# Optimization experiments

Measured on AMD Instinct MI355X. Metric: run time of the kernel, lower is better.

## Reference

```python
import jax, jax.numpy as jnp
import numpy as np

DIM = 768
NUM_HEADS = 12
HEAD_DIM = DIM // NUM_HEADS
SCALE = HEAD_DIM ** -0.5
H_IN, W_IN = 14, 14
N_TOK = H_IN * W_IN + 1  # 197 (patches + cls)
NUM_REL = (2 * H_IN - 1) * (2 * W_IN - 1) + 3  # 732
B = 128


def _build_rel_index():
    coords = np.stack(np.meshgrid(np.arange(H_IN), np.arange(W_IN), indexing='ij'))  # (2,H,W)
    flat = coords.reshape(2, -1)  # (2, H*W)
    rel = flat[:, :, None] - flat[:, None, :]  # (2, HW, HW)
    rel = rel.transpose(1, 2, 0).astype(np.int64)  # (HW, HW, 2)
    rel[:, :, 0] += H_IN - 1
    rel[:, :, 1] += W_IN - 1
    rel[:, :, 0] *= 2 * W_IN - 1
    idx = np.zeros((N_TOK, N_TOK), dtype=np.int64)
    idx[1:, 1:] = rel.sum(-1)
    idx[0, :] = NUM_REL - 3
    idx[:, 0] = NUM_REL - 2
    idx[0, 0] = NUM_REL - 1
    return jnp.asarray(idx, dtype=jnp.int32)


def binarize(x):
    # forward of STESign: -1 if x<0 else 1 (sign(0)->1)
    return jnp.where(x >= 0, 1.0, -1.0).astype(x.dtype)


def quantize_qk(x):
    # per-(B,H) mean-abs scale over token and head_dim axes, times sign
    s = jnp.mean(jnp.abs(x), axis=(-2, -1), keepdims=True)
    return s * binarize(x)


def round_ste(z):
    return z + jax.lax.stop_gradient(jnp.round(z) - z)


def quantize_p(x):
    qmax = 255.0
    s = 1.0 / qmax
    q = jnp.clip(round_ste(x / s), 0.0, qmax)
    return s * q


def quantize_v(x):
    # symmetric 8-bit quantization, channelwise over last dim, clip [-2,2]
    clipped = jnp.clip(x, -2.0, 2.0)
    max_in = jnp.max(jnp.abs(clipped), axis=-1, keepdims=True)
    s = (2.0 ** 7 - 1.0) / (max_in + 1e-8)
    return jnp.round(clipped * s) / s


def setup_inputs() -> dict:
    key = jax.random.key(0)
    ks = jax.random.split(key, 5)
    x = jax.random.normal(ks[0], (B, N_TOK, DIM), dtype=jnp.float32)
    qkv_w = jax.random.normal(ks[1], (3 * DIM, DIM), dtype=jnp.float32) * (DIM ** -0.5)
    proj_w = jax.random.normal(ks[2], (DIM, DIM), dtype=jnp.float32) * (DIM ** -0.5)
    proj_b = jnp.zeros((DIM,), dtype=jnp.float32)
    rel_bias_table = jax.random.normal(ks[3], (NUM_REL, NUM_HEADS), dtype=jnp.float32) * 0.02
    rel_index = _build_rel_index()
    return {"x": x, "qkv_w": qkv_w, "proj_w": proj_w, "proj_b": proj_b,
            "rel_bias_table": rel_bias_table, "rel_index": rel_index}


def reference(x, qkv_w, proj_w, proj_b, rel_bias_table, rel_index):
    Bsz, N, C = x.shape
    qkv = x @ qkv_w.T  # (B,N,3C)
    qkv = qkv.reshape(Bsz, N, 3, NUM_HEADS, HEAD_DIM)
    qkv = jnp.transpose(qkv, (2, 0, 3, 1, 4))  # (3,B,H,N,hd)
    q, k, v = qkv[0], qkv[1], qkv[2]
    q = quantize_qk(q)
    k = quantize_qk(k)
    attn = jnp.einsum('bhnd,bhmd->bhnm', q, k) * SCALE  # (B,H,N,N)
    bias = rel_bias_table[rel_index]  # (N,N,H)
    attn = attn + jnp.transpose(bias, (2, 0, 1))[None]
    attn = jax.nn.softmax(attn, axis=-1)
    attn = quantize_p(attn)
    v = quantize_v(v)
    out = jnp.einsum('bhnm,bhmd->bhnd', attn, v)  # (B,H,N,hd)
    out = jnp.transpose(out, (0, 2, 1, 3)).reshape(Bsz, N, C)
    out = out @ proj_w.T + proj_b
    return out
```

## Files before the change

kernel.cpp:

```cpp
#include <hip/hip_runtime.h>
#include <cstdint>
#include <cmath>

#define NTOK 197
#define NHEAD 12
#define HD 64
#define CDIM 768
#define KPZ 200
#define VTS 256

typedef __attribute__((ext_vector_type(8))) short short8v;
typedef __attribute__((ext_vector_type(8))) _Float16 half8v;
typedef __attribute__((ext_vector_type(4))) float f32x4;

__device__ __forceinline__ unsigned short f2bf(float f) {
  unsigned u = __builtin_bit_cast(unsigned, f);
  unsigned r = (u + 0x7fffu + ((u >> 16) & 1u)) >> 16;
  return (unsigned short)r;
}
__device__ __forceinline__ float bf2f(unsigned short h) {
  unsigned u = ((unsigned)h) << 16;
  return __builtin_bit_cast(float, u);
}

__device__ __forceinline__ void gload_lds16(const unsigned short* g, unsigned short* l) {
  __builtin_amdgcn_global_load_lds(
      (const __attribute__((address_space(1))) unsigned int*)(const void*)g,
      (__attribute__((address_space(3))) unsigned int*)(void*)l, 16, 0, 0);
}

__global__ __launch_bounds__(256) void bias_pre_kernel(
    const float* __restrict__ table, const int* __restrict__ relidx,
    float* __restrict__ bias_pre, int total)
{
  int i = blockIdx.x * 256 + threadIdx.x;
  if (i >= total) return;
  int nm = i % (NTOK * NTOK);
  int h  = i / (NTOK * NTOK);
  bias_pre[i] = table[relidx[nm] * NHEAD + h];
}

__global__ __launch_bounds__(256) void split2h_kernel(
    const float* __restrict__ src,
    unsigned short* __restrict__ d0, unsigned short* __restrict__ d1,
    int Mreal, int C, long long total4)
{
  long long idx = (long long)blockIdx.x * 256 + threadIdx.x;
  if (idx >= total4) return;
  long long e = idx * 4;
  int r = (int)(e / C);
  float4 v = make_float4(0.f, 0.f, 0.f, 0.f);
  if (r < Mreal) v = *(const float4*)(src + e);
  const float vv[4] = {v.x, v.y, v.z, v.w};
  ushort4 o0, o1;
  unsigned short* p0 = (unsigned short*)&o0;
  unsigned short* p1 = (unsigned short*)&o1;
#pragma unroll
  for (int i = 0; i < 4; ++i) {
    const float t = vv[i] * 64.0f;
    const _Float16 h0 = (_Float16)t;
    const float rr = t - (float)h0;
    const _Float16 h1 = (_Float16)(rr * 4096.0f);
    p0[i] = __builtin_bit_cast(unsigned short, h0);
    p1[i] = __builtin_bit_cast(unsigned short, h1);
  }
  *(ushort4*)(d0 + e) = o0;
  *(ushort4*)(d1 + e) = o1;
}

template <int BANDW>
__global__ __launch_bounds__(256, 3) void gemm_f16(
    const unsigned short* __restrict__ A, size_t aplane,
    const unsigned short* __restrict__ B, size_t bplane,
    const float* __restrict__ bias, float* __restrict__ C,
    int M, int N, int K)
{
  __shared__ unsigned short Asm[2][128][64];
  __shared__ unsigned short Bsm[2][64][64];

  const int nwg = gridDim.x;
  const int orig = blockIdx.x;
  const int q = nwg >> 3, r = nwg & 7;
  const int xcd = orig & 7, pos = orig >> 3;
  const int wg = (xcd < r ? xcd * (q + 1) : r * (q + 1) + (xcd - r) * q) + pos;
  const int byCount = (M + 127) >> 7;
  const int bandSz = byCount * BANDW;
  const int band = wg / bandSz;
  const int rem = wg % bandSz;
  const int by = rem / BANDW;
  const int bx = band * BANDW + rem % BANDW;
  const int bm = by * 128, bn = bx * 64;

  const int tid = threadIdx.x;
  const int w = tid >> 6, lane = tid & 63;
  const int wr = w >> 1, wc = w & 1;
  const int srow = tid >> 3;
  const int sslot = tid & 7;
  const int sgW = (sslot ^ (srow & 7)) * 8;
  const int fr = lane & 15;
  const int fq = lane >> 4;
  const int mrow = wr * 64 + fr;
  const int ncol = wc * 32;
  const int kc0 = 8 * ((fq) ^ (fr & 7));
  const int kc1 = 8 * ((4 + fq) ^ (fr & 7));

  size_t aoffs[4], boffs[2];
#pragma unroll
  for (int ps = 0; ps < 4; ++ps) aoffs[ps] = (size_t)(bm + srow + 32 * ps) * K + sgW;
#pragma unroll
  for (int ps = 0; ps < 2; ++ps) boffs[ps] = (size_t)(bn + srow + 32 * ps) * K + sgW;

  f32x4 accA[4][2], accB[4][2];
#pragma unroll
  for (int i = 0; i < 4; ++i)
#pragma unroll
    for (int j = 0; j < 2; ++j) {
      accA[i][j] = (f32x4){0.f, 0.f, 0.f, 0.f};
      accB[i][j] = (f32x4){0.f, 0.f, 0.f, 0.f};
    }

  auto stage = [&](int k0) {
#pragma unroll
    for (int ps = 0; ps < 4; ++ps) {
      const int dr = srow + 32 * ps;
      gload_lds16(A + aoffs[ps] + k0,          &Asm[0][dr][sslot * 8]);
      gload_lds16(A + aplane + aoffs[ps] + k0, &Asm[1][dr][sslot * 8]);
    }
#pragma unroll
    for (int ps = 0; ps < 2; ++ps) {
      const int dr = srow + 32 * ps;
      gload_lds16(B + boffs[ps] + k0,          &Bsm[0][dr][sslot * 8]);
      gload_lds16(B + bplane + boffs[ps] + k0, &Bsm[1][dr][sslot * 8]);
    }
  };

  stage(0);
  __syncthreads();

#pragma unroll 1
  for (int k0 = 0; k0 < K; k0 += 64) {
    {
      half8v b0[2], b1[2];
#pragma unroll
      for (int nt = 0; nt < 2; ++nt) {
        b0[nt] = *(const half8v*)&Bsm[0][ncol + nt * 16 + fr][kc0];
        b1[nt] = *(const half8v*)&Bsm[1][ncol + nt * 16 + fr][kc0];
      }
#pragma unroll
      for (int mt = 0; mt < 4; ++mt) {
        const half8v a0 = *(const half8v*)&Asm[0][mrow + mt * 16][kc0];
        const half8v a1 = *(const half8v*)&Asm[1][mrow + mt * 16][kc0];
#pragma unroll
        for (int nt = 0; nt < 2; ++nt)
          accA[mt][nt] = __builtin_amdgcn_mfma_f32_16x16x32_f16(
              a0, b0[nt], accA[mt][nt], 0, 0, 0);
#pragma unroll
        for (int nt = 0; nt < 2; ++nt)
          accB[mt][nt] = __builtin_amdgcn_mfma_f32_16x16x32_f16(
              a0, b1[nt], accB[mt][nt], 0, 0, 0);
#pragma unroll
        for (int nt = 0; nt < 2; ++nt)
          accB[mt][nt] = __builtin_amdgcn_mfma_f32_16x16x32_f16(
              a1, b0[nt], accB[mt][nt], 0, 0, 0);
      }
    }
    {
      half8v a0[4], a1[4], b0[2], b1[2];
#pragma unroll
      for (int mt = 0; mt < 4; ++mt) {
        a0[mt] = *(const half8v*)&Asm[0][mrow + mt * 16][kc1];
        a1[mt] = *(const half8v*)&Asm[1][mrow + mt * 16][kc1];
      }
#pragma unroll
      for (int nt = 0; nt < 2; ++nt) {
        b0[nt] = *(const half8v*)&Bsm[0][ncol + nt * 16 + fr][kc1];
        b1[nt] = *(const half8v*)&Bsm[1][ncol + nt * 16 + fr][kc1];
      }
      __syncthreads();
      if (k0 + 64 < K) stage(k0 + 64);
      __builtin_amdgcn_sched_barrier(0);
#pragma unroll
      for (int mt = 0; mt < 4; ++mt)
#pragma unroll
        for (int nt = 0; nt < 2; ++nt)
          accA[mt][nt] = __builtin_amdgcn_mfma_f32_16x16x32_f16(
              a0[mt], b0[nt], accA[mt][nt], 0, 0, 0);
#pragma unroll
      for (int mt = 0; mt < 4; ++mt)
#pragma unroll
        for (int nt = 0; nt < 2; ++nt)
          accB[mt][nt] = __builtin_amdgcn_mfma_f32_16x16x32_f16(
              a0[mt], b1[nt], accB[mt][nt], 0, 0, 0);
#pragma unroll
      for (int mt = 0; mt < 4; ++mt)
#pragma unroll
        for (int nt = 0; nt < 2; ++nt)
          accB[mt][nt] = __builtin_amdgcn_mfma_f32_16x16x32_f16(
              a1[mt], b0[nt], accB[mt][nt], 0, 0, 0);
    }
    __syncthreads();
  }

  constexpr float S1 = 1.0f / 4096.0f;
#pragma unroll
  for (int nt = 0; nt < 2; ++nt) {
    const int col = bn + wc * 32 + nt * 16 + fr;
    const float bcol = bias ? bias[col] : 0.0f;
#pragma unroll
    for (int mt = 0; mt < 4; ++mt) {
      const int rowbase = bm + wr * 64 + mt * 16 + fq * 4;
#pragma unroll
      for (int j = 0; j < 4; ++j) {
        const int row = rowbase + j;
        if (row < M)
          C[(size_t)row * N + col] =
              (accA[mt][nt][j] + accB[mt][nt][j] * S1) * S1 + bcol;
      }
    }
  }
}

__global__ __launch_bounds__(512, 4) void attn_kernel(
    const float* __restrict__ qkv, const float* __restrict__ bias_pre,
    unsigned short* __restrict__ att0, unsigned short* __restrict__ att1)
{
  __shared__ unsigned short vT[2][HD][VTS];
  __shared__ unsigned char  zb[32][KPZ];
  __shared__ unsigned long long qb[200];
  __shared__ unsigned long long kbt[200];
  __shared__ float red[16];

  const int bh = blockIdx.x;
  const int b = bh / NHEAD;
  const int h = bh % NHEAD;
  const int tid = threadIdx.x;
  const int w = tid >> 6;
  const int lane = tid & 63;
  const float* base = qkv + (size_t)b * (NTOK * 3 * CDIM) + h * HD;

  float sq = 0.f, sk = 0.f;
  for (int n = w; n < NTOK; n += 8) {
    const float* row = base + (size_t)n * (3 * CDIM);
    const float qv = row[lane];
    const float kv = row[CDIM + lane];
    const float vv = row[2 * CDIM + lane];
    sq += fabsf(qv);
    sk += fabsf(kv);
    const unsigned long long qm = __ballot(qv >= 0.0f);
    const unsigned long long km = __ballot(kv >= 0.0f);
    if (lane == 0) { qb[n] = qm; kbt[n] = km; }
    const float c = fminf(fmaxf(vv, -2.0f), 2.0f);
    float a = fabsf(c);
#pragma unroll
    for (int off = 32; off; off >>= 1) a = fmaxf(a, __shfl_xor(a, off));
    const float s = 127.0f / (a + 1e-8f);
    const float vq = rintf(c * s) / s;
    const unsigned short l0 = f2bf(vq);
    const unsigned short l1 = f2bf(vq - bf2f(l0));
    const int gsw = ((((n >> 3) ^ (lane & 31)) << 3) | (n & 7));
    vT[0][lane][gsw] = l0;
    vT[1][lane][gsw] = l1;
  }
#pragma unroll
  for (int off = 32; off; off >>= 1) {
    sq += __shfl_xor(sq, off);
    sk += __shfl_xor(sk, off);
  }
  if (lane == 0) { red[w] = sq; red[8 + w] = sk; }
  __syncthreads();
  float s_q = 0.f, s_k = 0.f;
#pragma unroll
  for (int i = 0; i < 8; ++i) { s_q += red[i]; s_k += red[8 + i]; }
  s_q *= (1.0f / (NTOK * HD));
  s_k *= (1.0f / (NTOK * HD));
  const float coef = s_q * s_k * 0.125f;

  const float* biash = bias_pre + (size_t)h * (NTOK * NTOK);
  const float SP = 1.0f / 255.0f;

  const int mt = w >> 2;
  const int nt = w & 3;
  const int arow = mt * 16 + (lane & 15);
  const int bcol = nt * 16 + (lane & 15);
  const int kq8 = 8 * (lane >> 4);
  const int rowb = mt * 16 + ((lane >> 4) << 2);
  const int colOut = h * HD + bcol;
  const int bsw = bcol & 31;

  for (int g = 0; g < 7; ++g) {
    const int r0 = g * 32;

#pragma unroll
    for (int i = 0; i < 4; ++i) {
      const int r = r0 + w * 4 + i;
      if (r < NTOK) {
        const unsigned long long qn = qb[r];
        const float* brow = biash + (size_t)r * NTOK;
        float lg[4];
#pragma unroll
        for (int t = 0; t < 4; ++t) {
          const int m = lane + t * 64;
          if (m < NTOK) {
            const int dot = 64 - 2 * __popcll(qn ^ kbt[m]);
            lg[t] = fmaf(coef, (float)dot, brow[m]);
          } else {
            lg[t] = -INFINITY;
          }
        }
        float mx = fmaxf(fmaxf(lg[0], lg[1]), fmaxf(lg[2], lg[3]));
#pragma unroll
        for (int off = 32; off; off >>= 1) mx = fmaxf(mx, __shfl_xor(mx, off));
        const float p0 = expf(lg[0] - mx);
        const float p1 = expf(lg[1] - mx);
        const float p2 = expf(lg[2] - mx);
        const float p3 = expf(lg[3] - mx);
        float sum = p0 + p1 + p2 + p3;
#pragma unroll
        for (int off = 32; off; off >>= 1) sum += __shfl_xor(sum, off);
        float z0 = rintf((p0 / sum) / SP); z0 = fminf(fmaxf(z0, 0.f), 255.f);
        float z1 = rintf((p1 / sum) / SP); z1 = fminf(fmaxf(z1, 0.f), 255.f);
        float z2 = rintf((p2 / sum) / SP); z2 = fminf(fmaxf(z2, 0.f), 255.f);
        float z3 = rintf((p3 / sum) / SP); z3 = fminf(fmaxf(z3, 0.f), 255.f);
        const int zr = w * 4 + i;
        zb[zr][lane]       = (unsigned char)(int)z0;
        zb[zr][lane + 64]  = (unsigned char)(int)z1;
        zb[zr][lane + 128] = (unsigned char)(int)z2;
        if (lane + 192 < NTOK) zb[zr][lane + 192] = (unsigned char)(int)z3;
      }
    }
    __syncthreads();

    f32x4 acc = (f32x4){0.f, 0.f, 0.f, 0.f};
#pragma unroll
    for (int k0 = 0; k0 < 192; k0 += 32) {
      const unsigned long long a8 =
          *(const unsigned long long*)&zb[arow][k0 + kq8];
      short8v af;
#pragma unroll
      for (int j = 0; j < 8; ++j) {
        const float f = (float)((unsigned)(a8 >> (8 * j)) & 0xFFu);
        af[j] = (short)(__builtin_bit_cast(unsigned, f) >> 16);
      }
      const int kg = (((k0 + kq8) >> 3) ^ bsw) << 3;
      const short8v b0 = *(const short8v*)&vT[0][bcol][kg];
      const short8v b1 = *(const short8v*)&vT[1][bcol][kg];
      acc = __builtin_amdgcn_mfma_f32_16x16x32_bf16(af, b0, acc, 0, 0, 0);
      acc = __builtin_amdgcn_mfma_f32_16x16x32_bf16(af, b1, acc, 0, 0, 0);
    }
#pragma unroll
    for (int j = 0; j < 4; ++j) {
      float a = acc[j];
#pragma unroll
      for (int m = 192; m < 197; ++m) {
        const int mg = ((((m >> 3) ^ bsw) << 3) | (m & 7));
        const float zv = (float)zb[rowb + j][m];
        const float vv = bf2f(vT[0][bcol][mg]) + bf2f(vT[1][bcol][mg]);
        a = fmaf(zv, vv, a);
      }
      acc[j] = a;
    }
#pragma unroll
    for (int j = 0; j < 4; ++j) {
      const int row = r0 + rowb + j;
      if (row < NTOK) {
        const size_t off = ((size_t)b * NTOK + row) * CDIM + colOut;
        const float t = acc[j] * SP * 64.0f;
        const _Float16 h0 = (_Float16)t;
        const float rr = t - (float)h0;
        const _Float16 h1 = (_Float16)(rr * 4096.0f);
        att0[off] = __builtin_bit_cast(unsigned short, h0);
        att1[off] = __builtin_bit_cast(unsigned short, h1);
      }
    }
    __syncthreads();
  }
}

extern "C" void kernel_launch(void* const* d_in, const int* in_sizes, int n_in,
                              void* d_out, int out_size, void* d_ws, size_t ws_size,
                              hipStream_t stream)
{
  (void)in_sizes; (void)n_in; (void)out_size;
  const float* x      = (const float*)d_in[0];
  const float* qkv_w  = (const float*)d_in[1];
  const float* proj_w = (const float*)d_in[2];
  const float* proj_b = (const float*)d_in[3];
  const float* table  = (const float*)d_in[4];
  const int*   relidx = (const int*)d_in[5];
  float* out = (float*)d_out;

  const size_t biasElems = (size_t)NHEAD * NTOK * NTOK;
  const size_t wqPlane = (size_t)(3 * CDIM) * CDIM;
  const size_t wpPlane = (size_t)CDIM * CDIM;

  int nb = 128;
  size_t Mpad = 0;
  for (;; nb >>= 1) {
    size_t Mreal = (size_t)nb * NTOK;
    Mpad = (Mreal + 127) & ~(size_t)127;
    size_t need = biasElems * 4 + (2 * wqPlane + 2 * wpPlane) * 2 +
                  2 * Mpad * CDIM * 2 +
                  Mreal * (size_t)(3 * CDIM) * 4;
    if (need <= ws_size || nb == 1) break;
  }

  char* p = (char*)d_ws;
  float* bias_pre = (float*)p;               p += biasElems * 4;
  unsigned short* wq = (unsigned short*)p;   p += 2 * wqPlane * 2;
  unsigned short* wp = (unsigned short*)p;   p += 2 * wpPlane * 2;
  unsigned short* xs = (unsigned short*)p;   p += 2 * Mpad * CDIM * 2;
  float* qkvbuf = (float*)p;

  const size_t xPlane = Mpad * CDIM;

  {
    const int total = (int)biasElems;
    bias_pre_kernel<<<(total + 255) / 256, 256, 0, stream>>>(table, relidx, bias_pre, total);
  }
  {
    long long t4 = (long long)(3 * CDIM) * CDIM / 4;
    split2h_kernel<<<(int)((t4 + 255) / 256), 256, 0, stream>>>(
        qkv_w, wq, wq + wqPlane, 3 * CDIM, CDIM, t4);
    t4 = (long long)CDIM * CDIM / 4;
    split2h_kernel<<<(int)((t4 + 255) / 256), 256, 0, stream>>>(
        proj_w, wp, wp + wpPlane, CDIM, CDIM, t4);
  }

  for (int b0 = 0; b0 < 128; b0 += nb) {
    const int curB = (128 - b0 < nb) ? (128 - b0) : nb;
    const int Mreal = curB * NTOK;
    {
      long long t4 = (long long)Mpad * CDIM / 4;
      split2h_kernel<<<(int)((t4 + 255) / 256), 256, 0, stream>>>(
          x + (size_t)b0 * NTOK * CDIM, xs, xs + xPlane, Mreal, CDIM, t4);
    }
    const int mtiles = (int)(Mpad / 128);
    gemm_f16<18><<<mtiles * 36, 256, 0, stream>>>(
        xs, xPlane, wq, wqPlane, nullptr, qkvbuf, Mreal, 3 * CDIM, CDIM);
    attn_kernel<<<curB * NHEAD, 512, 0, stream>>>(qkvbuf, bias_pre, xs, xs + xPlane);
    gemm_f16<12><<<mtiles * 12, 256, 0, stream>>>(
        xs, xPlane, wp, wpPlane, proj_b, out + (size_t)b0 * NTOK * CDIM,
        Mreal, CDIM, CDIM);
  }
}
```

Baseline: 776.8 us.

## Double-buffer GEMM LDS tiles with K-step 32 and prefetch next tile

Restructures the split-fp16 GEMM main loop from a single 64-wide K tile, whose reload waited on an intra-iteration barrier, to a double-buffered 32-wide K tile. The load for the next tile is issued into the alternate buffer at the start of each iteration, overlapping global-to-LDS traffic with MFMA work. The swizzle is adapted to 32-column rows, and s_setprio is raised around the MFMA block. The LDS footprint is unchanged, but there are twice as many loop iterations and barriers, and each wave issues fewer loads per step.

```diff
diff --git a/kernel.cpp b/kernel.cpp
--- a/kernel.cpp
+++ b/kernel.cpp
@@ -75,8 +75,8 @@
     const float* __restrict__ bias, float* __restrict__ C,
     int M, int N, int K)
 {
-  __shared__ unsigned short Asm[2][128][64];
-  __shared__ unsigned short Bsm[2][64][64];
+  __shared__ unsigned short Asm[2][2][128][32];
+  __shared__ unsigned short Bsm[2][2][64][32];
 
   const int nwg = gridDim.x;
   const int orig = blockIdx.x;
@@ -94,21 +94,18 @@
   const int tid = threadIdx.x;
   const int w = tid >> 6, lane = tid & 63;
   const int wr = w >> 1, wc = w & 1;
-  const int srow = tid >> 3;
-  const int sslot = tid & 7;
-  const int sgW = (sslot ^ (srow & 7)) * 8;
+  const int sr = tid >> 2, gi = tid & 3;
+  const int sgW = (gi ^ ((sr >> 1) & 3)) * 8;
+  const int scW = gi * 8;
   const int fr = lane & 15;
   const int fq = lane >> 4;
   const int mrow = wr * 64 + fr;
   const int ncol = wc * 32;
-  const int kc0 = 8 * ((fq) ^ (fr & 7));
-  const int kc1 = 8 * ((4 + fq) ^ (fr & 7));
-
-  size_t aoffs[4], boffs[2];
-#pragma unroll
-  for (int ps = 0; ps < 4; ++ps) aoffs[ps] = (size_t)(bm + srow + 32 * ps) * K + sgW;
-#pragma unroll
-  for (int ps = 0; ps < 2; ++ps) boffs[ps] = (size_t)(bn + srow + 32 * ps) * K + sgW;
+  const int kcsw = 8 * (fq ^ ((fr >> 1) & 3));
+
+  const size_t aoff0 = (size_t)(bm + sr) * K + sgW;
+  const size_t aoff1 = (size_t)(bm + sr + 64) * K + sgW;
+  const size_t boff  = (size_t)(bn + sr) * K + sgW;
 
   f32x4 accA[4][2], accB[4][2];
 #pragma unroll
@@ -119,85 +116,57 @@
       accB[i][j] = (f32x4){0.f, 0.f, 0.f, 0.f};
     }
 
-  auto stage = [&](int k0) {
-#pragma unroll
-    for (int ps = 0; ps < 4; ++ps) {
-      const int dr = srow + 32 * ps;
-      gload_lds16(A + aoffs[ps] + k0,          &Asm[0][dr][sslot * 8]);
-      gload_lds16(A + aplane + aoffs[ps] + k0, &Asm[1][dr][sslot * 8]);
-    }
-#pragma unroll
-    for (int ps = 0; ps < 2; ++ps) {
-      const int dr = srow + 32 * ps;
-      gload_lds16(B + boffs[ps] + k0,          &Bsm[0][dr][sslot * 8]);
-      gload_lds16(B + bplane + boffs[ps] + k0, &Bsm[1][dr][sslot * 8]);
+  auto stage = [&](int buf, int k0) {
+#pragma unroll
+    for (int p = 0; p < 2; ++p) {
+      const unsigned short* Ap = A + (size_t)p * aplane + k0;
+      gload_lds16(Ap + aoff0, &Asm[buf][p][sr][scW]);
+      gload_lds16(Ap + aoff1, &Asm[buf][p][sr + 64][scW]);
+      gload_lds16(B + (size_t)p * bplane + k0 + boff, &Bsm[buf][p][sr & 63][scW]);
     }
   };
 
-  stage(0);
+  const int NT = K >> 5;
+
+  stage(0, 0);
   __syncthreads();
 
 #pragma unroll 1
-  for (int k0 = 0; k0 < K; k0 += 64) {
-    {
-      half8v b0[2], b1[2];
-#pragma unroll
-      for (int nt = 0; nt < 2; ++nt) {
-        b0[nt] = *(const half8v*)&Bsm[0][ncol + nt * 16 + fr][kc0];
-        b1[nt] = *(const half8v*)&Bsm[1][ncol + nt * 16 + fr][kc0];
-      }
-#pragma unroll
-      for (int mt = 0; mt < 4; ++mt) {
-        const half8v a0 = *(const half8v*)&Asm[0][mrow + mt * 16][kc0];
-        const half8v a1 = *(const half8v*)&Asm[1][mrow + mt * 16][kc0];
-#pragma unroll
-        for (int nt = 0; nt < 2; ++nt)
-          accA[mt][nt] = __builtin_amdgcn_mfma_f32_16x16x32_f16(
-              a0, b0[nt], accA[mt][nt], 0, 0, 0);
-#pragma unroll
-        for (int nt = 0; nt < 2; ++nt)
-          accB[mt][nt] = __builtin_amdgcn_mfma_f32_16x16x32_f16(
-              a0, b1[nt], accB[mt][nt], 0, 0, 0);
-#pragma unroll
-        for (int nt = 0; nt < 2; ++nt)
-          accB[mt][nt] = __builtin_amdgcn_mfma_f32_16x16x32_f16(
-              a1, b0[nt], accB[mt][nt], 0, 0, 0);
-      }
-    }
-    {
-      half8v a0[4], a1[4], b0[2], b1[2];
-#pragma unroll
-      for (int mt = 0; mt < 4; ++mt) {
-        a0[mt] = *(const half8v*)&Asm[0][mrow + mt * 16][kc1];
-        a1[mt] = *(const half8v*)&Asm[1][mrow + mt * 16][kc1];
-      }
-#pragma unroll
-      for (int nt = 0; nt < 2; ++nt) {
-        b0[nt] = *(const half8v*)&Bsm[0][ncol + nt * 16 + fr][kc1];
-        b1[nt] = *(const half8v*)&Bsm[1][ncol + nt * 16 + fr][kc1];
-      }
-      __syncthreads();
-      if (k0 + 64 < K) stage(k0 + 64);
-      __builtin_amdgcn_sched_barrier(0);
-#pragma unroll
-      for (int mt = 0; mt < 4; ++mt)
-#pragma unroll
-        for (int nt = 0; nt < 2; ++nt)
-          accA[mt][nt] = __builtin_amdgcn_mfma_f32_16x16x32_f16(
-              a0[mt], b0[nt], accA[mt][nt], 0, 0, 0);
-#pragma unroll
-      for (int mt = 0; mt < 4; ++mt)
-#pragma unroll
-        for (int nt = 0; nt < 2; ++nt)
-          accB[mt][nt] = __builtin_amdgcn_mfma_f32_16x16x32_f16(
-              a0[mt], b1[nt], accB[mt][nt], 0, 0, 0);
-#pragma unroll
-      for (int mt = 0; mt < 4; ++mt)
-#pragma unroll
-        for (int nt = 0; nt < 2; ++nt)
-          accB[mt][nt] = __builtin_amdgcn_mfma_f32_16x16x32_f16(
-              a1[mt], b0[nt], accB[mt][nt], 0, 0, 0);
-    }
+  for (int kt = 0; kt < NT; ++kt) {
+    const int cur = kt & 1;
+    if (kt + 1 < NT) stage(cur ^ 1, (kt + 1) * 32);
+    __builtin_amdgcn_sched_barrier(0);
+    half8v a0[4], a1[4], b0[2], b1[2];
+#pragma unroll
+    for (int mt = 0; mt < 4; ++mt) {
+      a0[mt] = *(const half8v*)&Asm[cur][0][mrow + mt * 16][kcsw];
+      a1[mt] = *(const half8v*)&Asm[cur][1][mrow + mt * 16][kcsw];
+    }
+#pragma unroll
+    for (int nt = 0; nt < 2; ++nt) {
+      b0[nt] = *(const half8v*)&Bsm[cur][0][ncol + nt * 16 + fr][kcsw];
+      b1[nt] = *(const half8v*)&Bsm[cur][1][ncol + nt * 16 + fr][kcsw];
+    }
+    __builtin_amdgcn_s_setprio(1);
+#pragma unroll
+    for (int mt = 0; mt < 4; ++mt)
+#pragma unroll
+      for (int nt = 0; nt < 2; ++nt)
+        accA[mt][nt] = __builtin_amdgcn_mfma_f32_16x16x32_f16(
+            a0[mt], b0[nt], accA[mt][nt], 0, 0, 0);
+#pragma unroll
+    for (int mt = 0; mt < 4; ++mt)
+#pragma unroll
+      for (int nt = 0; nt < 2; ++nt)
+        accB[mt][nt] = __builtin_amdgcn_mfma_f32_16x16x32_f16(
+            a0[mt], b1[nt], accB[mt][nt], 0, 0, 0);
+#pragma unroll
+    for (int mt = 0; mt < 4; ++mt)
+#pragma unroll
+      for (int nt = 0; nt < 2; ++nt)
+        accB[mt][nt] = __builtin_amdgcn_mfma_f32_16x16x32_f16(
+            a1[mt], b0[nt], accB[mt][nt], 0, 0, 0);
+    __builtin_amdgcn_s_setprio(0);
     __syncthreads();
   }
 
```

Result: slower. 919.8 us (+18.4%).
